# Optimization experiments

Measured on AMD Instinct MI355X. Metric: run time of the kernel, lower is better.

The kernel has to match this reference:

```python
import jax, jax.numpy as jnp
import numpy as np
from jax import lax

HEADS = 8
AGENT = 49            # agent_num
POOL = 7              # int(sqrt(agent_num))
DOWN_H, DOWN_W = 7, 7  # downstream_agent_shape
DIM = 256
WIN = 56              # sqrt(num_patches)


def _resize(x, oh, ow):
    # torch F.interpolate(mode='bilinear', align_corners=False) equivalent for upsample/identity
    return jax.image.resize(x, x.shape[:-2] + (oh, ow), method='bilinear', antialias=False)


def _bias_pipeline(bias, H, W):
    # bias: (heads, AGENT, h0, w0) -> (heads, H*W, DOWN_H*DOWN_W)
    h = bias.shape[0]
    pb = _resize(bias, H, W)                                     # (h, 49, H, W)
    pb = pb.reshape(h, POOL, POOL, H * W).transpose(0, 3, 1, 2)  # (h, HW, 7, 7)
    pb = _resize(pb, DOWN_H, DOWN_W)                             # (h, HW, 7, 7)
    return pb.reshape(h, H * W, DOWN_H * DOWN_W)


def setup_inputs() -> dict:
    key = jax.random.key(0)
    ks = jax.random.split(key, 16)
    b, H, W = 16, WIN, WIN
    n, c, h = H * W, DIM, HEADS
    s = 0.02
    f32 = jnp.float32
    return {
        "x": jax.random.normal(ks[0], (b, n, c), f32),
        "H": H,
        "W": W,
        "Wq": jax.random.normal(ks[1], (c, c), f32) * c ** -0.5,
        "Wkv": jax.random.normal(ks[2], (2 * c, c), f32) * c ** -0.5,
        "Wproj": jax.random.normal(ks[3], (c, c), f32) * c ** -0.5,
        "bproj": jnp.zeros((c,), f32),
        "dwc_w": jax.random.normal(ks[4], (c, 1, 3, 3), f32) * 0.1,
        "dwc_b": jnp.zeros((c,), f32),
        "an_bias": jax.random.normal(ks[5], (h, AGENT, 7, 7), f32) * s,
        "na_bias": jax.random.normal(ks[6], (h, AGENT, 7, 7), f32) * s,
        "ah_bias": jax.random.normal(ks[7], (1, h, AGENT, WIN, 1), f32) * s,
        "aw_bias": jax.random.normal(ks[8], (1, h, AGENT, 1, WIN), f32) * s,
        "ha_bias": jax.random.normal(ks[9], (1, h, WIN, 1, AGENT), f32) * s,
        "wa_bias": jax.random.normal(ks[10], (1, h, 1, WIN, AGENT), f32) * s,
    }


def reference(x, H, W, Wq, Wkv, Wproj, bproj, dwc_w, dwc_b,
              an_bias, na_bias, ah_bias, aw_bias, ha_bias, wa_bias):
    b, n, c = x.shape
    h = HEADS
    hd = c // h
    T = n // 2
    scale = hd ** -0.5
    dan = DOWN_H * DOWN_W

    q_lin = x @ Wq.T                       # (b,n,c)
    kv = x @ Wkv.T                         # (b,n,2c)
    k_lin, v_lin = kv[..., :c], kv[..., c:]

    # adaptive avg pool of q to (7,7) agent grid (H, W divisible by 7)
    qg = q_lin.reshape(b, DOWN_H, H // DOWN_H, DOWN_W, W // DOWN_W, c).mean(axis=(2, 4))
    agent = qg.reshape(b, dan, h, hd).transpose(0, 2, 1, 3)   # (b,h,49,hd)

    q = q_lin.reshape(b, n, h, hd).transpose(0, 2, 1, 3)      # (b,h,n,hd)
    k = k_lin.reshape(b, n, h, hd).transpose(0, 2, 1, 3)
    v = v_lin.reshape(b, n, h, hd).transpose(0, 2, 1, 3)

    # agent -> kv attention biases
    pb1 = _bias_pipeline(an_bias, H, W).transpose(0, 2, 1)    # (h,49,HW)
    pb2 = _bias_pipeline((ah_bias + aw_bias)[0], H, W).transpose(0, 2, 1)
    position_bias = (pb1 + pb2)[None]                         # (1,h,49,HW)

    agent_attn = jax.nn.softmax(
        jnp.einsum('bhad,bhnd->bhan', agent * scale, k) + position_bias, axis=-1)
    agent_v = jnp.einsum('bhan,bhnd->bhad', agent_attn, v)    # (b,h,49,hd)

    # query -> agent attention biases
    ab1 = _bias_pipeline(na_bias, H, W)                       # (h,HW,49)
    ab2 = _bias_pipeline((ha_bias + wa_bias)[0].transpose(0, 3, 1, 2), H, W)
    agent_bias = (ab1 + ab2)[None]                            # (1,h,HW,49)

    # top-T query selection, then bilinear upsample of scores back to n rows
    token_w = jax.nn.softmax(q.mean(axis=-1), axis=-1)        # (b,h,n)
    _, top_idx = lax.top_k(token_w, T)                        # (b,h,T)
    q_top = jnp.take_along_axis(q, top_idx[..., None], axis=2)  # (b,h,T,hd)
    q2 = jnp.einsum('bhtd,bhad->bhta', q_top, agent)          # (b,h,T,49)
    q2 = _resize(q2, n, dan) * scale                          # (b,h,n,49)

    q_attn = jax.nn.softmax(q2 + agent_bias, axis=-1)
    out = jnp.einsum('bhna,bhad->bhnd', q_attn, agent_v)
    out = out.transpose(0, 2, 1, 3).reshape(b, n, c)

    # depthwise conv branch on v
    v_img = v.transpose(0, 2, 1, 3).reshape(b, H, W, c).transpose(0, 3, 1, 2)  # (b,c,H,W)
    dw = lax.conv_general_dilated(v_img, dwc_w, (1, 1), ((1, 1), (1, 1)),
                                  feature_group_count=c)
    dw = dw + dwc_b[None, :, None, None]
    out = out + dw.transpose(0, 2, 3, 1).reshape(b, n, c)
    return out @ Wproj.T + bproj
```

## Files before the change

kernel.cpp:

```cpp
#include <hip/hip_runtime.h>
#include <stdint.h>

typedef _Float16 f16;
typedef _Float16 half8 __attribute__((ext_vector_type(8)));
typedef float f32x4 __attribute__((ext_vector_type(4)));

#define NBATCH 16
#define NTOK 3136
#define NTOT 50176
#define NH 8
#define NA 49
#define NAP 64
#define TTOP 1568
#define NTILES 196
#define PBH 200704
#define SCALE 0.17677669529663687f
#define FPARTS 4

__device__ __forceinline__ f32x4 mfma16(half8 a, half8 b, f32x4 c) {
  return __builtin_amdgcn_mfma_f32_16x16x32_f16(a, b, c, 0, 0, 0);
}

__device__ __forceinline__ void gload16(const void* g, void* l) {
  __builtin_amdgcn_global_load_lds(
      (const __attribute__((address_space(1))) void*)g,
      (__attribute__((address_space(3))) void*)l, 16, 0, 0);
}

__global__ __launch_bounds__(256) void k_prep_w(const float* Wq, const float* Wkv, const float* Wproj,
                                                f16* wqkv, f16* wproj) {
  int total1 = 768 * 256;
  int total = total1 + 256 * 256;
  for (int i = blockIdx.x * 256 + threadIdx.x; i < total; i += gridDim.x * 256) {
    if (i < total1) {
      int j = i >> 8, k = i & 255;
      float v = (j < 256) ? Wq[j * 256 + k] : Wkv[(j - 256) * 256 + k];
      wqkv[i] = (f16)v;
    } else {
      int i2 = i - total1;
      wproj[i2] = (f16)Wproj[i2];
    }
  }
}

__global__ __launch_bounds__(256) void k_cvt_x(const float* x, f16* xh, long total) {
  long i = (long)blockIdx.x * blockDim.x + threadIdx.x;
  long stride = (long)gridDim.x * blockDim.x;
  for (long e = i * 8; e < total; e += stride * 8) {
    float4 v0 = *(const float4*)(x + e);
    float4 v1 = *(const float4*)(x + e + 4);
    half8 o = {(f16)v0.x, (f16)v0.y, (f16)v0.z, (f16)v0.w,
               (f16)v1.x, (f16)v1.y, (f16)v1.z, (f16)v1.w};
    *(half8*)(xh + e) = o;
  }
}

__global__ __launch_bounds__(256) void k_bias(const float* an_b, const float* na_b,
                                              const float* ah_b, const float* aw_b,
                                              const float* ha_b, const float* wa_b,
                                              float* pos_bias, float* agent_bias) {
  int n = blockIdx.x * 256 + threadIdx.x;
  int h = blockIdx.y;
  if (n >= NTOK) return;
  int y = n / 56, x = n - y * 56;
  float py = (y + 0.5f) * 0.125f - 0.5f;
  float px = (x + 0.5f) * 0.125f - 0.5f;
  int iy0 = (int)floorf(py); float fy = py - (float)iy0;
  int ix0 = (int)floorf(px); float fx = px - (float)ix0;
  int y0 = max(iy0, 0), y1 = min(iy0 + 1, 6);
  int x0 = max(ix0, 0), x1 = min(ix0 + 1, 6);
  float w00 = (1.f - fy) * (1.f - fx), w01 = (1.f - fy) * fx;
  float w10 = fy * (1.f - fx), w11 = fy * fx;
  for (int a = 0; a < NA; ++a) {
    const float* pa = an_b + (h * NA + a) * 49;
    float up_an = w00 * pa[y0 * 7 + x0] + w01 * pa[y0 * 7 + x1] +
                  w10 * pa[y1 * 7 + x0] + w11 * pa[y1 * 7 + x1];
    const float* pn = na_b + (h * NA + a) * 49;
    float up_na = w00 * pn[y0 * 7 + x0] + w01 * pn[y0 * 7 + x1] +
                  w10 * pn[y1 * 7 + x0] + w11 * pn[y1 * 7 + x1];
    float pb = up_an + ah_b[(h * NA + a) * 56 + y] + aw_b[(h * NA + a) * 56 + x];
    pos_bias[((size_t)(h * NAP + a)) * NTOK + n] = pb;
    float ab = up_na + ha_b[(h * 56 + y) * NA + a] + wa_b[(h * 56 + x) * NA + a];
    agent_bias[((size_t)(h * NAP + a)) * NTOK + n] = ab;
  }
  for (int a = NA; a < NAP; ++a)
    pos_bias[((size_t)(h * NAP + a)) * NTOK + n] = 0.f;
}

template <bool PROJ>
__global__ __launch_bounds__(256) void k_gemm(const f16* __restrict__ A, const f16* __restrict__ Bw,
                                              f16* __restrict__ CH, float* __restrict__ Cf32,
                                              const float* __restrict__ bias, int N) {
  __shared__ __align__(16) char lds[16384];
  int per = gridDim.x >> 3;
  int wrk = (blockIdx.x & 7) * per + (blockIdx.x >> 3);
  int nNT = N >> 7;
  int mt = wrk / nNT, nt = wrk - mt * nNT;
  int m0 = mt * 128, n0 = nt * 128;
  int tid = threadIdx.x, w = tid >> 6, l = tid & 63, lr = l & 15, lg = l >> 4;
  int wm = w >> 1, wn = w & 1;
  f32x4 acc[4][4] = {};
  const char* Bb = (const char*)Bw + (size_t)n0 * 512;
  int rowA0 = 32 * w + (l >> 2);
  int rowA1 = rowA0 + 16;
  int koff = (l & 3) * 16;
  char* ldsA0 = lds + (2 * w) * 1024;
  char* ldsA1 = lds + (2 * w + 1) * 1024;
  char* ldsB0 = lds + 8192 + (2 * w) * 1024;
  char* ldsB1 = lds + 8192 + (2 * w + 1) * 1024;

  for (int k0 = 0; k0 < 256; k0 += 32) {
    if (PROJ) {
      const char* Ab = (const char*)A + ((size_t)(k0 >> 5) * NTOT + m0) * 64;
      gload16(Ab + (size_t)rowA0 * 64 + koff, ldsA0);
      gload16(Ab + (size_t)rowA1 * 64 + koff, ldsA1);
    } else {
      const char* Ab = (const char*)A + (size_t)m0 * 512 + k0 * 2;
      gload16(Ab + (size_t)rowA0 * 512 + koff, ldsA0);
      gload16(Ab + (size_t)rowA1 * 512 + koff, ldsA1);
    }
    gload16(Bb + (size_t)rowA0 * 512 + k0 * 2 + koff, ldsB0);
    gload16(Bb + (size_t)rowA1 * 512 + k0 * 2 + koff, ldsB1);
    __syncthreads();
    half8 af[4], bf[4];
#pragma unroll
    for (int m4 = 0; m4 < 4; ++m4) {
      int row = wm * 64 + m4 * 16 + lr;
      af[m4] = *(const half8*)(lds + row * 64 + lg * 16);
    }
#pragma unroll
    for (int n4 = 0; n4 < 4; ++n4) {
      int row = wn * 64 + n4 * 16 + lr;
      bf[n4] = *(const half8*)(lds + 8192 + row * 64 + lg * 16);
    }
#pragma unroll
    for (int m4 = 0; m4 < 4; ++m4)
#pragma unroll
      for (int n4 = 0; n4 < 4; ++n4)
        acc[m4][n4] = mfma16(af[m4], bf[n4], acc[m4][n4]);
    __syncthreads();
  }

  if (PROJ) {
#pragma unroll
    for (int n4 = 0; n4 < 4; ++n4) {
      int n = n0 + wn * 64 + n4 * 16 + lr;
#pragma unroll
      for (int m4 = 0; m4 < 4; ++m4)
#pragma unroll
        for (int r = 0; r < 4; ++r) {
          int m = m0 + wm * 64 + m4 * 16 + lg * 4 + r;
          Cf32[(size_t)m * N + n] = acc[m4][n4][r] + bias[n];
        }
    }
  } else {
    f16* cl = (f16*)lds;
    int rr = tid >> 2, c4 = tid & 3;
#pragma unroll
    for (int hm = 0; hm < 2; ++hm) {
      __syncthreads();
      if (wm == hm) {
#pragma unroll
        for (int m4 = 0; m4 < 4; ++m4)
#pragma unroll
          for (int n4 = 0; n4 < 4; ++n4)
#pragma unroll
            for (int r = 0; r < 4; ++r)
              cl[(m4 * 16 + lg * 4 + r) * 128 + wn * 64 + n4 * 16 + lr] = (f16)acc[m4][n4][r];
      }
      __syncthreads();
#pragma unroll
      for (int cc = 0; cc < 4; ++cc) {
        int pn = (n0 >> 5) + cc;
        half8 v = *(const half8*)(cl + rr * 128 + cc * 32 + c4 * 8);
        *(half8*)(CH + ((size_t)pn * NTOT + m0 + hm * 64 + rr) * 32 + c4 * 8) = v;
      }
    }
  }
}

__global__ __launch_bounds__(256) void k_pool_tw(const f16* qkvH, f16* agent, float* tw) {
  int bh = blockIdx.x, b = bh >> 3, h = bh & 7;
  int tid = threadIdx.x;
  const f16* qp0 = qkvH + ((size_t)h * NTOT + (size_t)b * NTOK) * 32;
  {
    int a = tid >> 2, c = tid & 3;
    float s8[8] = {};
    if (a < NA) {
      int dh = a / 7, dwi = a - dh * 7;
      for (int i = 0; i < 8; ++i)
#pragma unroll
        for (int j = 0; j < 8; ++j) {
          int tok = (dh * 8 + i) * 56 + dwi * 8 + j;
          half8 v = *(const half8*)(qp0 + (size_t)tok * 32 + c * 8);
#pragma unroll
          for (int e = 0; e < 8; ++e) s8[e] += (float)v[e];
        }
    }
    half8 o;
#pragma unroll
    for (int e = 0; e < 8; ++e) o[e] = (f16)(s8[e] * (SCALE / 64.f));
    *(half8*)(agent + (size_t)bh * NAP * 32 + a * 32 + c * 8) = o;
  }
  for (int n = tid; n < NTOK; n += 256) {
    const half8* qp = (const half8*)(qp0 + (size_t)n * 32);
    float sum = 0.f;
#pragma unroll
    for (int j = 0; j < 4; ++j) {
      half8 v = qp[j];
#pragma unroll
      for (int e = 0; e < 8; ++e) sum += (float)v[e];
    }
    tw[(size_t)bh * NTOK + n] = sum * (1.f / 32.f);
  }
}

template <int J>
__device__ __forceinline__ void stage_local(unsigned long long (&key)[16], int kmask, int base) {
#pragma unroll
  for (int e = 0; e < 16; ++e) {
    if ((e & J) == 0) {
      bool desc = (((base + e) & kmask) == 0);
      unsigned long long a = key[e], c = key[e | J];
      if ((a < c) == desc) { key[e] = c; key[e | J] = a; }
    }
  }
}

__global__ __launch_bounds__(256, 1) void k_topk(const float* tw, int* topidx) {
  __shared__ unsigned long long lk[4096 + 256];
  int bh = blockIdx.x, tid = threadIdx.x;
  const float* p = tw + (size_t)bh * NTOK;
  unsigned long long key[16];
  int base = tid * 16;
#pragma unroll
  for (int e = 0; e < 16; ++e) {
    int s = base + e;
    float v = (s < NTOK) ? p[s] : -1e30f;
    unsigned ub = __float_as_uint(v);
    ub = (ub & 0x80000000u) ? ~ub : (ub | 0x80000000u);
    unsigned low = (s < NTOK) ? ~(unsigned)s : 0u;
    key[e] = ((unsigned long long)ub << 32) | low;
  }
  stage_local<1>(key, 2, base);
  stage_local<2>(key, 4, base);  stage_local<1>(key, 4, base);
  stage_local<4>(key, 8, base);  stage_local<2>(key, 8, base);  stage_local<1>(key, 8, base);
  stage_local<8>(key, 16, base); stage_local<4>(key, 16, base);
  stage_local<2>(key, 16, base); stage_local<1>(key, 16, base);
  for (int k = 32; k <= 4096; k <<= 1) {
    bool desc = ((base & k) == 0);
    for (int j = k >> 1; j >= 16; j >>= 1) {
      int m = j >> 4;
      bool takeMax = (((tid & m) == 0) == desc);
      unsigned long long pv[16];
      if (m <= 32) {
#pragma unroll
        for (int e = 0; e < 16; ++e) pv[e] = __shfl_xor(key[e], m, 64);
      } else {
        __syncthreads();
#pragma unroll
        for (int e = 0; e < 16; ++e) { int ix = base + e; lk[ix + (ix >> 4)] = key[e]; }
        __syncthreads();
        int pb = (tid ^ m) * 16;
#pragma unroll
        for (int e = 0; e < 16; ++e) { int ix = pb + e; pv[e] = lk[ix + (ix >> 4)]; }
      }
#pragma unroll
      for (int e = 0; e < 16; ++e)
        key[e] = takeMax ? (key[e] > pv[e] ? key[e] : pv[e])
                         : (key[e] < pv[e] ? key[e] : pv[e]);
    }
    stage_local<8>(key, k, base);
    stage_local<4>(key, k, base);
    stage_local<2>(key, k, base);
    stage_local<1>(key, k, base);
  }
  if (tid < TTOP / 16) {
    int* op = topidx + (size_t)bh * TTOP + base;
#pragma unroll
    for (int e = 0; e < 16; ++e) op[e] = (int)(~(unsigned)key[e]);
  }
}

__global__ __launch_bounds__(256) void k_vt(const f16* qkvH, f16* vt) {
  __shared__ __align__(16) f16 t[64][40];
  int bh = blockIdx.y, b = bh >> 3, h = bh & 7;
  int n0 = blockIdx.x * 64;
  int tid = threadIdx.x;
  const f16* vp = qkvH + ((size_t)(16 + h) * NTOT + (size_t)b * NTOK + n0) * 32;
  {
    int nl = tid >> 2, c = tid & 3;
    *(half8*)(&t[nl][c * 8]) = *(const half8*)(vp + (size_t)nl * 32 + c * 8);
  }
  __syncthreads();
  for (int s = tid; s < 64 * 32; s += 256) {
    int d = s >> 6, nl = s & 63;
    vt[((size_t)(bh * 32 + d)) * NTOK + n0 + nl] = t[nl][d];
  }
}

__global__ __launch_bounds__(256) void k_flash(const f16* qkvH, const f16* agent, const f16* vt,
                                               const float* pos_bias, float* opart, float* rspart) {
  __shared__ __align__(16) f16 pbuf[4][64][40];
  __shared__ float ored[64][33];
  __shared__ float rssum[64];
  int part = blockIdx.x, bh = blockIdx.y, b = bh >> 3, h = bh & 7;
  int tid = threadIdx.x, w = tid >> 6, l = tid & 63, lr = l & 15, lg = l >> 4;
  half8 afrag[4];
#pragma unroll
  for (int mt = 0; mt < 4; ++mt)
    afrag[mt] = *(const half8*)(agent + ((size_t)bh * 64 + mt * 16 + lr) * 32 + lg * 8);
  f32x4 o[4][2] = {};
  float rs[4][4] = {};
  const f16* kbase = qkvH + ((size_t)(8 + h) * NTOT + (size_t)b * NTOK) * 32;
  const f16* vtb = vt + (size_t)bh * 32 * NTOK;
  const float* pbb = pos_bias + (size_t)h * NAP * NTOK;
  f32x4 zero = {};
  for (int n0 = (part * 4 + w) * 32; n0 < NTOK; n0 += 512) {
#pragma unroll
    for (int t2 = 0; t2 < 2; ++t2) {
      int nc = n0 + t2 * 16;
      half8 kf = *(const half8*)(kbase + (size_t)(nc + lr) * 32 + lg * 8);
#pragma unroll
      for (int mt = 0; mt < 4; ++mt) {
        f32x4 s = mfma16(afrag[mt], kf, zero);
#pragma unroll
        for (int r = 0; r < 4; ++r) {
          int a = mt * 16 + lg * 4 + r;
          float pv = __expf(s[r] + pbb[(size_t)a * NTOK + nc + lr]);
          rs[mt][r] += pv;
          pbuf[w][a][t2 * 16 + lr] = (f16)pv;
        }
      }
    }
    half8 pf[4];
#pragma unroll
    for (int mt = 0; mt < 4; ++mt)
      pf[mt] = *(const half8*)(&pbuf[w][mt * 16 + lr][lg * 8]);
#pragma unroll
    for (int dt = 0; dt < 2; ++dt) {
      half8 vf = *(const half8*)(vtb + (size_t)(dt * 16 + lr) * NTOK + n0 + lg * 8);
#pragma unroll
      for (int mt = 0; mt < 4; ++mt)
        o[mt][dt] = mfma16(pf[mt], vf, o[mt][dt]);
    }
  }
#pragma unroll
  for (int mt = 0; mt < 4; ++mt)
#pragma unroll
    for (int r = 0; r < 4; ++r) {
      float v = rs[mt][r];
      for (int off = 1; off < 16; off <<= 1) v += __shfl_xor(v, off, 64);
      rs[mt][r] = v;
    }
  for (int s = tid; s < 64 * 33; s += 256) ((float*)ored)[s] = 0.f;
  if (tid < 64) rssum[tid] = 0.f;
  __syncthreads();
  for (int ww = 0; ww < 4; ++ww) {
    if (w == ww) {
      if (lr == 0)
#pragma unroll
        for (int mt = 0; mt < 4; ++mt)
#pragma unroll
          for (int r = 0; r < 4; ++r) rssum[mt * 16 + lg * 4 + r] += rs[mt][r];
#pragma unroll
      for (int mt = 0; mt < 4; ++mt)
#pragma unroll
        for (int dt = 0; dt < 2; ++dt)
#pragma unroll
          for (int r = 0; r < 4; ++r)
            ored[mt * 16 + lg * 4 + r][dt * 16 + lr] += o[mt][dt][r];
    }
    __syncthreads();
  }
  int pp = bh * FPARTS + part;
  for (int s = tid; s < NA * 32; s += 256) {
    int a = s >> 5, d = s & 31;
    opart[((size_t)pp * 64 + a) * 32 + d] = ored[a][d];
  }
  if (tid < NA) rspart[(size_t)pp * 64 + tid] = rssum[tid];
}

__global__ __launch_bounds__(256) void k_fred(const float* opart, const float* rspart, float* agv) {
  int bh = blockIdx.x, tid = threadIdx.x;
  for (int s = tid; s < NA * 32; s += 256) {
    int a = s >> 5, d = s & 31;
    float o = 0.f, rs = 0.f;
#pragma unroll
    for (int p = 0; p < FPARTS; ++p) {
      int pp = bh * FPARTS + p;
      o += opart[((size_t)pp * 64 + a) * 32 + d];
      rs += rspart[(size_t)pp * 64 + a];
    }
    agv[(size_t)bh * NA * 32 + s] = o / rs;
  }
}

__global__ __launch_bounds__(256) void k_psm(const f16* qkvH, const f16* agent, const int* topidx,
                                             const float* agent_bias, f16* P) {
  __shared__ __align__(16) f16 q2buf[144][88];
  int chunk = blockIdx.x, bh = blockIdx.y, b = bh >> 3, h = bh & 7;
  int tid = threadIdx.x, w = tid >> 6, l = tid & 63, lr = l & 15, lg = l >> 4;
  const f16* qplane = qkvH + ((size_t)h * NTOT + (size_t)b * NTOK) * 32;
  half8 bfrag[4];
#pragma unroll
  for (int nt = 0; nt < 4; ++nt)
    bfrag[nt] = *(const half8*)(agent + ((size_t)bh * 64 + nt * 16 + lr) * 32 + lg * 8);
  int jbase = chunk * 128 - 8;
  f32x4 zero = {};
  for (int mt = w; mt < 9; mt += 4) {
    int j = jbase + mt * 16 + lr;
    int jc = min(max(j, 0), TTOP - 1);
    int tok = topidx[(size_t)bh * TTOP + jc];
    half8 qf = *(const half8*)(qplane + (size_t)tok * 32 + lg * 8);
#pragma unroll
    for (int nt = 0; nt < 4; ++nt) {
      f32x4 s = mfma16(qf, bfrag[nt], zero);
#pragma unroll
      for (int r = 0; r < 4; ++r)
        q2buf[mt * 16 + lg * 4 + r][nt * 16 + lr] = (f16)s[r];
    }
  }
  __syncthreads();
  int g = chunk * 256 + tid;
  if (g >= NTOK) return;
  int hi = g >> 1;
  int jA, jB; float wAq, wBq;
  if (g & 1) { jA = hi; jB = hi + 1; wAq = 0.75f; wBq = 0.25f; }
  else       { jA = hi - 1; jB = hi; wAq = 0.25f; wBq = 0.75f; }
  jA = min(max(jA, 0), TTOP - 1);
  jB = min(max(jB, 0), TTOP - 1);
  int lA = jA - jbase, lB = jB - jbase;
  const float* ab = agent_bias + (size_t)h * NAP * NTOK + g;
  f16* Pb = P + (size_t)bh * PBH;
  int tile = g >> 4, lrr = g & 15;
  float ssum = 0.f;
  half8 oo[7];
#pragma unroll
  for (int c = 0; c < 7; ++c) {
    half8 a8 = *(const half8*)(&q2buf[lA][c * 8]);
    half8 b8 = *(const half8*)(&q2buf[lB][c * 8]);
#pragma unroll
    for (int e = 0; e < 8; ++e) {
      int a = c * 8 + e;
      float pv = 0.f;
      if (a < NA) {
        float v = wAq * (float)a8[e] + wBq * (float)b8[e] + ab[(size_t)a * NTOK];
        pv = __expf(v);
        ssum += pv;
      }
      oo[c][e] = (f16)pv;
    }
  }
  f16 invs = (f16)(1.f / ssum);
  half8 iv8 = {invs, invs, invs, invs, invs, invs, invs, invs};
#pragma unroll
  for (int c = 0; c < 7; ++c)
    *(half8*)(Pb + ((size_t)(tile * 8 + c) * 16 + lrr) * 8) = oo[c] * iv8;
  half8 z = {};
  *(half8*)(Pb + ((size_t)(tile * 8 + 7) * 16 + lrr) * 8) = z;
}

__global__ __launch_bounds__(256) void k_out(const f16* __restrict__ P,
                                             const float* __restrict__ agent_v,
                                             const f16* __restrict__ qkvH,
                                             const float* __restrict__ dwc_w,
                                             const float* __restrict__ dwc_b,
                                             f16* __restrict__ preH) {
  __shared__ __align__(16) f16 avT[32][72];
  __shared__ __align__(16) f16 ctile[224][40];
  __shared__ float wconv[9][32];
  __shared__ float bconv[32];
  int chunk = blockIdx.x, bh = blockIdx.y, b = bh >> 3, h = bh & 7;
  int tid = threadIdx.x, w = tid >> 6, l = tid & 63, lr = l & 15, lg = l >> 4;
  int y0 = chunk * 4;
  const f16* vp = qkvH + ((size_t)(16 + h) * NTOT + (size_t)b * NTOK) * 32;
  const f16* Pb = P + (size_t)bh * PBH;
  half8 pa0[4], pa1[4];
#pragma unroll
  for (int i = 0; i < 4; ++i) {
    int lt = w * 4 + i;
    if (lt < 14) {
      const f16* Pt = Pb + (size_t)(chunk * 14 + lt) * 1024;
      pa0[i] = *(const half8*)(Pt + ((size_t)(0 + lg) * 16 + lr) * 8);
      pa1[i] = *(const half8*)(Pt + ((size_t)(4 + lg) * 16 + lr) * 8);
    }
  }
  for (int s = tid; s < 32 * 64; s += 256) {
    int d = s >> 6, a = s & 63;
    avT[d][a] = (a < NA) ? (f16)agent_v[((size_t)bh * NA + a) * 32 + d] : (f16)0.f;
  }
  for (int s = tid; s < 32 * 9; s += 256) {
    int d = s / 9, t = s - d * 9;
    wconv[t][d] = dwc_w[(size_t)(h * 32 + d) * 9 + t];
  }
  if (tid < 32) bconv[tid] = dwc_b[h * 32 + tid];
  __syncthreads();
  half8 bf[2][2];
#pragma unroll
  for (int nt = 0; nt < 2; ++nt)
#pragma unroll
    for (int ks = 0; ks < 2; ++ks)
      bf[nt][ks] = *(const half8*)(&avT[0][0] + (size_t)(nt * 16 + lr) * 72 + ks * 32 + lg * 8);
#pragma unroll
  for (int i = 0; i < 4; ++i) {
    int lt = w * 4 + i;
    if (lt >= 14) continue;
    f32x4 acc0 = {}, acc1 = {};
    acc0 = mfma16(pa0[i], bf[0][0], acc0);
    acc0 = mfma16(pa1[i], bf[0][1], acc0);
    acc1 = mfma16(pa0[i], bf[1][0], acc1);
    acc1 = mfma16(pa1[i], bf[1][1], acc1);
    int ltrow = lt * 16 + lg * 4;
#pragma unroll
    for (int r = 0; r < 4; ++r) {
      ctile[ltrow + r][lr] = (f16)acc0[r];
      ctile[ltrow + r][16 + lr] = (f16)acc1[r];
    }
  }
  __syncthreads();
  if (tid >= 224) return;
  int g = chunk * 224 + tid;
  int ly = tid / 56, x = tid - ly * 56;
  int y = y0 + ly;
  float accd[32];
#pragma unroll
  for (int c = 0; c < 4; ++c) {
    half8 cv = *(const half8*)(&ctile[tid][c * 8]);
#pragma unroll
    for (int e = 0; e < 8; ++e) accd[c * 8 + e] = (float)cv[e] + bconv[c * 8 + e];
  }
#pragma unroll
  for (int ky = 0; ky < 3; ++ky) {
    int gy = y + ky - 1;
    if (gy < 0 || gy >= 56) continue;
#pragma unroll
    for (int kx = 0; kx < 3; ++kx) {
      int xx = x + kx - 1;
      if (xx < 0 || xx >= 56) continue;
      int t = ky * 3 + kx;
      const f16* vt9 = vp + (size_t)(gy * 56 + xx) * 32;
#pragma unroll
      for (int c = 0; c < 4; ++c) {
        half8 vv = *(const half8*)(vt9 + c * 8);
#pragma unroll
        for (int e = 0; e < 8; ++e) accd[c * 8 + e] += wconv[t][c * 8 + e] * (float)vv[e];
      }
    }
  }
  f16* op = preH + ((size_t)h * NTOT + (size_t)b * NTOK + g) * 32;
#pragma unroll
  for (int c = 0; c < 4; ++c) {
    half8 o;
#pragma unroll
    for (int e = 0; e < 8; ++e) o[e] = (f16)accd[c * 8 + e];
    *(half8*)(op + c * 8) = o;
  }
}

extern "C" void kernel_launch(void* const* d_in, const int* in_sizes, int n_in,
                              void* d_out, int out_size, void* d_ws, size_t ws_size,
                              hipStream_t stream) {
  const float* x     = (const float*)d_in[0];
  const float* Wq    = (const float*)d_in[3];
  const float* Wkv   = (const float*)d_in[4];
  const float* Wproj = (const float*)d_in[5];
  const float* bproj = (const float*)d_in[6];
  const float* dwc_w = (const float*)d_in[7];
  const float* dwc_b = (const float*)d_in[8];
  const float* an_b  = (const float*)d_in[9];
  const float* na_b  = (const float*)d_in[10];
  const float* ah_b  = (const float*)d_in[11];
  const float* aw_b  = (const float*)d_in[12];
  const float* ha_b  = (const float*)d_in[13];
  const float* wa_b  = (const float*)d_in[14];

  char* ws = (char*)d_ws;
  size_t off = 0;
  auto alloc = [&](size_t bytes) {
    void* p = ws + off;
    off = (off + bytes + 255) & ~(size_t)255;
    return p;
  };
  f16* wqkv    = (f16*)alloc((size_t)768 * 256 * 2);
  f16* wproj   = (f16*)alloc((size_t)256 * 256 * 2);
  f16* qkvH    = (f16*)alloc((size_t)24 * NTOT * 32 * 2);
  float* posb  = (float*)alloc((size_t)8 * NAP * NTOK * 4);
  float* agb   = (float*)alloc((size_t)8 * NAP * NTOK * 4);
  f16* agent   = (f16*)alloc((size_t)128 * NAP * 32 * 2);
  float* tw    = (float*)alloc((size_t)128 * NTOK * 4);
  int* topidx  = (int*)alloc((size_t)128 * TTOP * 4);
  f16* vt      = (f16*)alloc((size_t)128 * 32 * NTOK * 2);
  float* agv   = (float*)alloc((size_t)128 * NA * 32 * 4);
  float* opart = (float*)alloc((size_t)128 * FPARTS * 64 * 32 * 4);
  float* rspart= (float*)alloc((size_t)128 * FPARTS * 64 * 4);
  f16* preH    = (f16*)alloc((size_t)8 * NTOT * 32 * 2);
  f16* P       = (f16*)alloc((size_t)128 * PBH * 2);
  f16* xh      = P;

  k_prep_w<<<1024, 256, 0, stream>>>(Wq, Wkv, Wproj, wqkv, wproj);
  k_cvt_x<<<2048, 256, 0, stream>>>(x, xh, (long)NTOT * 256);
  k_bias<<<dim3(13, 8), 256, 0, stream>>>(an_b, na_b, ah_b, aw_b, ha_b, wa_b, posb, agb);
  k_gemm<false><<<2352, 256, 0, stream>>>(xh, wqkv, qkvH, nullptr, nullptr, 768);
  k_pool_tw<<<128, 256, 0, stream>>>(qkvH, agent, tw);
  k_topk<<<128, 256, 0, stream>>>(tw, topidx);
  k_vt<<<dim3(49, 128), 256, 0, stream>>>(qkvH, vt);
  k_flash<<<dim3(FPARTS, 128), 256, 0, stream>>>(qkvH, agent, vt, posb, opart, rspart);
  k_fred<<<128, 256, 0, stream>>>(opart, rspart, agv);
  k_psm<<<dim3(13, 128), 256, 0, stream>>>(qkvH, agent, topidx, agb, P);
  k_out<<<dim3(14, 128), 256, 0, stream>>>(P, agv, qkvH, dwc_w, dwc_b, preH);
  k_gemm<true><<<784, 256, 0, stream>>>(preH, wproj, nullptr, (float*)d_out, bproj, 256);
}
```

Before: 245.6 us.

## Split top-k bitonic sort across two kernels and fuse softmax into output kernel

New measurement: 225.5 us. 8.2% less time.

```diff
diff --git a/kernel.cpp b/kernel.cpp
--- a/kernel.cpp
+++ b/kernel.cpp
@@ -12,8 +12,6 @@
 #define NA 49
 #define NAP 64
 #define TTOP 1568
-#define NTILES 196
-#define PBH 200704
 #define SCALE 0.17677669529663687f
 #define FPARTS 4
 
@@ -215,10 +213,10 @@
   }
 }
 
-template <int J>
-__device__ __forceinline__ void stage_local(unsigned long long (&key)[16], int kmask, int base) {
-#pragma unroll
-  for (int e = 0; e < 16; ++e) {
+template <int NE, int J>
+__device__ __forceinline__ void stage_local(unsigned long long (&key)[NE], int kmask, int base) {
+#pragma unroll
+  for (int e = 0; e < NE; ++e) {
     if ((e & J) == 0) {
       bool desc = (((base + e) & kmask) == 0);
       unsigned long long a = key[e], c = key[e | J];
@@ -227,54 +225,90 @@
   }
 }
 
-__global__ __launch_bounds__(256, 1) void k_topk(const float* tw, int* topidx) {
-  __shared__ unsigned long long lk[4096 + 256];
-  int bh = blockIdx.x, tid = threadIdx.x;
+__global__ __launch_bounds__(256, 1) void k_sort1(const float* tw, unsigned long long* keys64) {
+  __shared__ unsigned long long lk[2048 + 128];
+  int bh = blockIdx.x >> 1, half = blockIdx.x & 1;
+  int tid = threadIdx.x;
   const float* p = tw + (size_t)bh * NTOK;
-  unsigned long long key[16];
-  int base = tid * 16;
-#pragma unroll
-  for (int e = 0; e < 16; ++e) {
-    int s = base + e;
+  int gbase = half * 2048 + tid * 8;
+  unsigned long long key[8];
+#pragma unroll
+  for (int e = 0; e < 8; ++e) {
+    int s = gbase + e;
     float v = (s < NTOK) ? p[s] : -1e30f;
     unsigned ub = __float_as_uint(v);
     ub = (ub & 0x80000000u) ? ~ub : (ub | 0x80000000u);
     unsigned low = (s < NTOK) ? ~(unsigned)s : 0u;
     key[e] = ((unsigned long long)ub << 32) | low;
   }
-  stage_local<1>(key, 2, base);
-  stage_local<2>(key, 4, base);  stage_local<1>(key, 4, base);
-  stage_local<4>(key, 8, base);  stage_local<2>(key, 8, base);  stage_local<1>(key, 8, base);
-  stage_local<8>(key, 16, base); stage_local<4>(key, 16, base);
-  stage_local<2>(key, 16, base); stage_local<1>(key, 16, base);
-  for (int k = 32; k <= 4096; k <<= 1) {
-    bool desc = ((base & k) == 0);
-    for (int j = k >> 1; j >= 16; j >>= 1) {
-      int m = j >> 4;
+  stage_local<8, 1>(key, 2, gbase);
+  stage_local<8, 2>(key, 4, gbase); stage_local<8, 1>(key, 4, gbase);
+  stage_local<8, 4>(key, 8, gbase); stage_local<8, 2>(key, 8, gbase); stage_local<8, 1>(key, 8, gbase);
+  for (int k = 16; k <= 2048; k <<= 1) {
+    bool desc = ((gbase & k) == 0);
+    for (int j = k >> 1; j >= 8; j >>= 1) {
+      int m = j >> 3;
       bool takeMax = (((tid & m) == 0) == desc);
-      unsigned long long pv[16];
+      unsigned long long pv[8];
       if (m <= 32) {
 #pragma unroll
-        for (int e = 0; e < 16; ++e) pv[e] = __shfl_xor(key[e], m, 64);
+        for (int e = 0; e < 8; ++e) pv[e] = __shfl_xor(key[e], m, 64);
       } else {
         __syncthreads();
 #pragma unroll
-        for (int e = 0; e < 16; ++e) { int ix = base + e; lk[ix + (ix >> 4)] = key[e]; }
+        for (int e = 0; e < 8; ++e) { int ix = tid * 8 + e; lk[ix + (ix >> 4)] = key[e]; }
         __syncthreads();
-        int pb = (tid ^ m) * 16;
-#pragma unroll
-        for (int e = 0; e < 16; ++e) { int ix = pb + e; pv[e] = lk[ix + (ix >> 4)]; }
+        int pb = (tid ^ m) * 8;
+#pragma unroll
+        for (int e = 0; e < 8; ++e) { int ix = pb + e; pv[e] = lk[ix + (ix >> 4)]; }
       }
 #pragma unroll
-      for (int e = 0; e < 16; ++e)
+      for (int e = 0; e < 8; ++e)
         key[e] = takeMax ? (key[e] > pv[e] ? key[e] : pv[e])
                          : (key[e] < pv[e] ? key[e] : pv[e]);
     }
-    stage_local<8>(key, k, base);
-    stage_local<4>(key, k, base);
-    stage_local<2>(key, k, base);
-    stage_local<1>(key, k, base);
-  }
+    stage_local<8, 4>(key, k, gbase);
+    stage_local<8, 2>(key, k, gbase);
+    stage_local<8, 1>(key, k, gbase);
+  }
+  unsigned long long* op = keys64 + (size_t)bh * 4096 + gbase;
+#pragma unroll
+  for (int e = 0; e < 8; ++e) op[e] = key[e];
+}
+
+__global__ __launch_bounds__(256, 1) void k_sort2(const unsigned long long* keys64, int* topidx) {
+  __shared__ unsigned long long lk[4096 + 256];
+  int bh = blockIdx.x, tid = threadIdx.x;
+  const unsigned long long* ip = keys64 + (size_t)bh * 4096 + (size_t)tid * 16;
+  unsigned long long key[16];
+#pragma unroll
+  for (int e = 0; e < 16; ++e) key[e] = ip[e];
+  int base = tid * 16;
+  for (int j = 2048; j >= 16; j >>= 1) {
+    int m = j >> 4;
+    bool takeMax = ((tid & m) == 0);
+    unsigned long long pv[16];
+    if (m <= 32) {
+#pragma unroll
+      for (int e = 0; e < 16; ++e) pv[e] = __shfl_xor(key[e], m, 64);
+    } else {
+      __syncthreads();
+#pragma unroll
+      for (int e = 0; e < 16; ++e) { int ix = base + e; lk[ix + (ix >> 4)] = key[e]; }
+      __syncthreads();
+      int pb = (tid ^ m) * 16;
+#pragma unroll
+      for (int e = 0; e < 16; ++e) { int ix = pb + e; pv[e] = lk[ix + (ix >> 4)]; }
+    }
+#pragma unroll
+    for (int e = 0; e < 16; ++e)
+      key[e] = takeMax ? (key[e] > pv[e] ? key[e] : pv[e])
+                       : (key[e] < pv[e] ? key[e] : pv[e]);
+  }
+  stage_local<16, 8>(key, 4096, base);
+  stage_local<16, 4>(key, 4096, base);
+  stage_local<16, 2>(key, 4096, base);
+  stage_local<16, 1>(key, 4096, base);
   if (tid < TTOP / 16) {
     int* op = topidx + (size_t)bh * TTOP + base;
 #pragma unroll
@@ -396,19 +430,40 @@
   }
 }
 
-__global__ __launch_bounds__(256) void k_psm(const f16* qkvH, const f16* agent, const int* topidx,
-                                             const float* agent_bias, f16* P) {
-  __shared__ __align__(16) f16 q2buf[144][88];
+__global__ __launch_bounds__(256) void k_po(const f16* __restrict__ qkvH, const f16* __restrict__ agent,
+                                            const int* __restrict__ topidx,
+                                            const float* __restrict__ agent_bias,
+                                            const float* __restrict__ agent_v,
+                                            const float* __restrict__ dwc_w,
+                                            const float* __restrict__ dwc_b,
+                                            f16* __restrict__ preH) {
+  __shared__ __align__(16) char uq[18432];
+  __shared__ __align__(16) f16 pbuf[14 * 8 * 16 * 8];
+  __shared__ __align__(16) f16 avT[32][72];
+  __shared__ float wconv[9][32];
+  __shared__ float bconv[32];
+  f16 (*q2buf)[72] = (f16(*)[72])uq;
+  f16 (*ctile)[40] = (f16(*)[40])uq;
   int chunk = blockIdx.x, bh = blockIdx.y, b = bh >> 3, h = bh & 7;
   int tid = threadIdx.x, w = tid >> 6, l = tid & 63, lr = l & 15, lg = l >> 4;
   const f16* qplane = qkvH + ((size_t)h * NTOT + (size_t)b * NTOK) * 32;
+  const f16* vp = qkvH + ((size_t)(16 + h) * NTOT + (size_t)b * NTOK) * 32;
+  for (int s = tid; s < 32 * 64; s += 256) {
+    int d = s >> 6, a = s & 63;
+    avT[d][a] = (a < NA) ? (f16)agent_v[((size_t)bh * NA + a) * 32 + d] : (f16)0.f;
+  }
+  for (int s = tid; s < 32 * 9; s += 256) {
+    int d = s / 9, t = s - d * 9;
+    wconv[t][d] = dwc_w[(size_t)(h * 32 + d) * 9 + t];
+  }
+  if (tid < 32) bconv[tid] = dwc_b[h * 32 + tid];
   half8 bfrag[4];
 #pragma unroll
   for (int nt = 0; nt < 4; ++nt)
     bfrag[nt] = *(const half8*)(agent + ((size_t)bh * 64 + nt * 16 + lr) * 32 + lg * 8);
-  int jbase = chunk * 128 - 8;
+  int jbase = chunk * 112 - 8;
   f32x4 zero = {};
-  for (int mt = w; mt < 9; mt += 4) {
+  for (int mt = w; mt < 8; mt += 4) {
     int j = jbase + mt * 16 + lr;
     int jc = min(max(j, 0), TTOP - 1);
     int tok = topidx[(size_t)bh * TTOP + jc];
@@ -422,79 +477,43 @@
     }
   }
   __syncthreads();
-  int g = chunk * 256 + tid;
-  if (g >= NTOK) return;
-  int hi = g >> 1;
-  int jA, jB; float wAq, wBq;
-  if (g & 1) { jA = hi; jB = hi + 1; wAq = 0.75f; wBq = 0.25f; }
-  else       { jA = hi - 1; jB = hi; wAq = 0.25f; wBq = 0.75f; }
-  jA = min(max(jA, 0), TTOP - 1);
-  jB = min(max(jB, 0), TTOP - 1);
-  int lA = jA - jbase, lB = jB - jbase;
-  const float* ab = agent_bias + (size_t)h * NAP * NTOK + g;
-  f16* Pb = P + (size_t)bh * PBH;
-  int tile = g >> 4, lrr = g & 15;
-  float ssum = 0.f;
-  half8 oo[7];
-#pragma unroll
-  for (int c = 0; c < 7; ++c) {
-    half8 a8 = *(const half8*)(&q2buf[lA][c * 8]);
-    half8 b8 = *(const half8*)(&q2buf[lB][c * 8]);
-#pragma unroll
-    for (int e = 0; e < 8; ++e) {
-      int a = c * 8 + e;
-      float pv = 0.f;
-      if (a < NA) {
-        float v = wAq * (float)a8[e] + wBq * (float)b8[e] + ab[(size_t)a * NTOK];
-        pv = __expf(v);
-        ssum += pv;
+  if (tid < 224) {
+    int g = chunk * 224 + tid;
+    int hi = g >> 1;
+    int jA, jB; float wAq, wBq;
+    if (g & 1) { jA = hi; jB = hi + 1; wAq = 0.75f; wBq = 0.25f; }
+    else       { jA = hi - 1; jB = hi; wAq = 0.25f; wBq = 0.75f; }
+    jA = min(max(jA, 0), TTOP - 1);
+    jB = min(max(jB, 0), TTOP - 1);
+    int lA = jA - jbase, lB = jB - jbase;
+    const float* ab = agent_bias + (size_t)h * NAP * NTOK + g;
+    float ssum = 0.f;
+    half8 oo[7];
+#pragma unroll
+    for (int c = 0; c < 7; ++c) {
+      half8 a8 = *(const half8*)(&q2buf[lA][c * 8]);
+      half8 b8 = *(const half8*)(&q2buf[lB][c * 8]);
+#pragma unroll
+      for (int e = 0; e < 8; ++e) {
+        int a = c * 8 + e;
+        float pv = 0.f;
+        if (a < NA) {
+          float v = wAq * (float)a8[e] + wBq * (float)b8[e] + ab[(size_t)a * NTOK];
+          pv = __expf(v);
+          ssum += pv;
+        }
+        oo[c][e] = (f16)pv;
       }
-      oo[c][e] = (f16)pv;
-    }
-  }
-  f16 invs = (f16)(1.f / ssum);
-  half8 iv8 = {invs, invs, invs, invs, invs, invs, invs, invs};
-#pragma unroll
-  for (int c = 0; c < 7; ++c)
-    *(half8*)(Pb + ((size_t)(tile * 8 + c) * 16 + lrr) * 8) = oo[c] * iv8;
-  half8 z = {};
-  *(half8*)(Pb + ((size_t)(tile * 8 + 7) * 16 + lrr) * 8) = z;
-}
-
-__global__ __launch_bounds__(256) void k_out(const f16* __restrict__ P,
-                                             const float* __restrict__ agent_v,
-                                             const f16* __restrict__ qkvH,
-                                             const float* __restrict__ dwc_w,
-                                             const float* __restrict__ dwc_b,
-                                             f16* __restrict__ preH) {
-  __shared__ __align__(16) f16 avT[32][72];
-  __shared__ __align__(16) f16 ctile[224][40];
-  __shared__ float wconv[9][32];
-  __shared__ float bconv[32];
-  int chunk = blockIdx.x, bh = blockIdx.y, b = bh >> 3, h = bh & 7;
-  int tid = threadIdx.x, w = tid >> 6, l = tid & 63, lr = l & 15, lg = l >> 4;
-  int y0 = chunk * 4;
-  const f16* vp = qkvH + ((size_t)(16 + h) * NTOT + (size_t)b * NTOK) * 32;
-  const f16* Pb = P + (size_t)bh * PBH;
-  half8 pa0[4], pa1[4];
-#pragma unroll
-  for (int i = 0; i < 4; ++i) {
-    int lt = w * 4 + i;
-    if (lt < 14) {
-      const f16* Pt = Pb + (size_t)(chunk * 14 + lt) * 1024;
-      pa0[i] = *(const half8*)(Pt + ((size_t)(0 + lg) * 16 + lr) * 8);
-      pa1[i] = *(const half8*)(Pt + ((size_t)(4 + lg) * 16 + lr) * 8);
-    }
-  }
-  for (int s = tid; s < 32 * 64; s += 256) {
-    int d = s >> 6, a = s & 63;
-    avT[d][a] = (a < NA) ? (f16)agent_v[((size_t)bh * NA + a) * 32 + d] : (f16)0.f;
-  }
-  for (int s = tid; s < 32 * 9; s += 256) {
-    int d = s / 9, t = s - d * 9;
-    wconv[t][d] = dwc_w[(size_t)(h * 32 + d) * 9 + t];
-  }
-  if (tid < 32) bconv[tid] = dwc_b[h * 32 + tid];
+    }
+    f16 invs = (f16)(1.f / ssum);
+    half8 iv8 = {invs, invs, invs, invs, invs, invs, invs, invs};
+    int lt = tid >> 4, lrr = tid & 15;
+#pragma unroll
+    for (int c = 0; c < 7; ++c)
+      *(half8*)(pbuf + ((size_t)(lt * 8 + c) * 16 + lrr) * 8) = oo[c] * iv8;
+    half8 z = {};
+    *(half8*)(pbuf + ((size_t)(lt * 8 + 7) * 16 + lrr) * 8) = z;
+  }
   __syncthreads();
   half8 bf[2][2];
 #pragma unroll
@@ -506,11 +525,13 @@
   for (int i = 0; i < 4; ++i) {
     int lt = w * 4 + i;
     if (lt >= 14) continue;
+    half8 pa0 = *(const half8*)(pbuf + ((size_t)(lt * 8 + lg) * 16 + lr) * 8);
+    half8 pa1 = *(const half8*)(pbuf + ((size_t)(lt * 8 + 4 + lg) * 16 + lr) * 8);
     f32x4 acc0 = {}, acc1 = {};
-    acc0 = mfma16(pa0[i], bf[0][0], acc0);
-    acc0 = mfma16(pa1[i], bf[0][1], acc0);
-    acc1 = mfma16(pa0[i], bf[1][0], acc1);
-    acc1 = mfma16(pa1[i], bf[1][1], acc1);
+    acc0 = mfma16(pa0, bf[0][0], acc0);
+    acc0 = mfma16(pa1, bf[0][1], acc0);
+    acc1 = mfma16(pa0, bf[1][0], acc1);
+    acc1 = mfma16(pa1, bf[1][1], acc1);
     int ltrow = lt * 16 + lg * 4;
 #pragma unroll
     for (int r = 0; r < 4; ++r) {
@@ -521,6 +542,7 @@
   __syncthreads();
   if (tid >= 224) return;
   int g = chunk * 224 + tid;
+  int y0 = chunk * 4;
   int ly = tid / 56, x = tid - ly * 56;
   int y = y0 + ly;
   float accd[32];
@@ -590,24 +612,24 @@
   f16* agent   = (f16*)alloc((size_t)128 * NAP * 32 * 2);
   float* tw    = (float*)alloc((size_t)128 * NTOK * 4);
   int* topidx  = (int*)alloc((size_t)128 * TTOP * 4);
+  unsigned long long* keys64 = (unsigned long long*)alloc((size_t)128 * 4096 * 8);
   f16* vt      = (f16*)alloc((size_t)128 * 32 * NTOK * 2);
   float* agv   = (float*)alloc((size_t)128 * NA * 32 * 4);
   float* opart = (float*)alloc((size_t)128 * FPARTS * 64 * 32 * 4);
   float* rspart= (float*)alloc((size_t)128 * FPARTS * 64 * 4);
   f16* preH    = (f16*)alloc((size_t)8 * NTOT * 32 * 2);
-  f16* P       = (f16*)alloc((size_t)128 * PBH * 2);
-  f16* xh      = P;
+  f16* xh      = (f16*)alloc((size_t)NTOT * 256 * 2);
 
   k_prep_w<<<1024, 256, 0, stream>>>(Wq, Wkv, Wproj, wqkv, wproj);
   k_cvt_x<<<2048, 256, 0, stream>>>(x, xh, (long)NTOT * 256);
   k_bias<<<dim3(13, 8), 256, 0, stream>>>(an_b, na_b, ah_b, aw_b, ha_b, wa_b, posb, agb);
   k_gemm<false><<<2352, 256, 0, stream>>>(xh, wqkv, qkvH, nullptr, nullptr, 768);
   k_pool_tw<<<128, 256, 0, stream>>>(qkvH, agent, tw);
-  k_topk<<<128, 256, 0, stream>>>(tw, topidx);
+  k_sort1<<<256, 256, 0, stream>>>(tw, keys64);
+  k_sort2<<<128, 256, 0, stream>>>(keys64, topidx);
   k_vt<<<dim3(49, 128), 256, 0, stream>>>(qkvH, vt);
   k_flash<<<dim3(FPARTS, 128), 256, 0, stream>>>(qkvH, agent, vt, posb, opart, rspart);
   k_fred<<<128, 256, 0, stream>>>(opart, rspart, agv);
-  k_psm<<<dim3(13, 128), 256, 0, stream>>>(qkvH, agent, topidx, agb, P);
-  k_out<<<dim3(14, 128), 256, 0, stream>>>(P, agv, qkvH, dwc_w, dwc_b, preH);
+  k_po<<<dim3(14, 128), 256, 0, stream>>>(qkvH, agent, topidx, agb, agv, dwc_w, dwc_b, preH);
   k_gemm<true><<<784, 256, 0, stream>>>(preH, wproj, nullptr, (float*)d_out, bproj, 256);
 }
```
